# Kernel optimization log

Hardware: AMD Instinct MI355X
Metric: run time of the kernel (lower is better)

Reference implementation:

```python
import jax, jax.numpy as jnp
import numpy as np

H = 1024   # GRU hidden size
Z = 1024   # latent z dim
A = 4      # action dim
F = 30     # number of expert MLPs / max horizon
DIN = Z + H      # 2048, expert MLP input
DH = 512         # expert MLP hidden
EIN = H + 94     # evalMLP input (belief + pos/ori one-hot)
EH = 512
EOUT = 94


def setup_inputs() -> dict:
    key = jax.random.key(0)
    ks = jax.random.split(key, 20)
    s = 0.02
    inp = {
        "b_t": jax.random.normal(ks[0], (1, H), jnp.float32),
        "a_t": jax.random.normal(ks[1], (F, A), jnp.float32),
        "z_tp1_pos": jax.random.normal(ks[2], (F, Z), jnp.float32),
        "z_tp1_neg": jax.random.normal(ks[3], (F, Z), jnp.float32),
        "init_pos_ori": jax.random.uniform(ks[4], (1, 94), jnp.float32),
        # action GRU params (PyTorch layout: W_ih (3H, A), W_hh (3H, H))
        "gru_Wih": jax.random.normal(ks[5], (3 * H, A), jnp.float32) * s,
        "gru_Whh": jax.random.normal(ks[6], (3 * H, H), jnp.float32) * s,
        "gru_bih": jax.random.normal(ks[7], (3 * H,), jnp.float32) * s,
        "gru_bhh": jax.random.normal(ks[8], (3 * H,), jnp.float32) * s,
        # 30 stacked expert MLPs: Linear(DIN,DH)+ReLU+Linear(DH,1)
        "mlp_W1": jax.random.normal(ks[9], (F, DIN, DH), jnp.float32) * s,
        "mlp_b1": jax.random.normal(ks[10], (F, DH), jnp.float32) * s,
        "mlp_W2": jax.random.normal(ks[11], (F, DH, 1), jnp.float32) * s,
        "mlp_b2": jax.random.normal(ks[12], (F, 1), jnp.float32) * s,
        # evalMLP: Linear(EIN,EH)+ReLU+Linear(EH,EOUT)+sigmoid
        "eval_W1": jax.random.normal(ks[13], (EIN, EH), jnp.float32) * s,
        "eval_b1": jax.random.normal(ks[14], (EH,), jnp.float32) * s,
        "eval_W2": jax.random.normal(ks[15], (EH, EOUT), jnp.float32) * s,
        "eval_b2": jax.random.normal(ks[16], (EOUT,), jnp.float32) * s,
        "f": F,
    }
    return inp


def _gru(x, h0, Wih, Whh, bih, bhh):
    # x: (T, A), h0: (H,) -> outputs (T, H). PyTorch nn.GRU cell math.
    def step(h, xt):
        gi = Wih @ xt + bih          # (3H,)
        gh = Whh @ h + bhh           # (3H,)
        ir, iz, inn = jnp.split(gi, 3)
        hr, hz, hn = jnp.split(gh, 3)
        r = jax.nn.sigmoid(ir + hr)
        z = jax.nn.sigmoid(iz + hz)
        n = jnp.tanh(inn + r * hn)
        h_new = (1.0 - z) * n + z * h
        return h_new, h_new
    _, hs = jax.lax.scan(step, h0, x)
    return hs


def _experts(x, W1, b1, W2, b2, f):
    # x: (f, DIN); expert i applied to row i only (grouped batch-1 GEMMs).
    h = jax.nn.relu(jnp.einsum('fi,fih->fh', x, W1[:f]) + b1[:f])
    return jnp.einsum('fh,fho->fo', h, W2[:f]) + b2[:f]   # (f, 1) logits


def reference(b_t, a_t, z_tp1_pos, z_tp1_neg, init_pos_ori,
              gru_Wih, gru_Whh, gru_bih, gru_bhh,
              mlp_W1, mlp_b1, mlp_W2, mlp_b2,
              eval_W1, eval_b1, eval_W2, eval_b2, f):
    a_gru = _gru(a_t[:f], b_t[0], gru_Wih, gru_Whh, gru_bih, gru_bhh)  # (f, H)
    z_pos = jnp.concatenate([z_tp1_pos[:f], a_gru], axis=1)           # (f, Z+H)
    pred_positive = _experts(z_pos, mlp_W1, mlp_b1, mlp_W2, mlp_b2, f)
    z_neg = jnp.concatenate([z_tp1_neg[:f], a_gru], axis=1)
    pred_negative = _experts(z_neg, mlp_W1, mlp_b1, mlp_W2, mlp_b2, f)
    # eval branch uses b_t.detach()
    eval_in = jnp.concatenate([jax.lax.stop_gradient(b_t), init_pos_ori], axis=1)
    eh = jax.nn.relu(eval_in @ eval_W1 + eval_b1)
    pred_xytheta = jax.nn.sigmoid(eh @ eval_W2 + eval_b2)             # (1, 94)
    return pred_positive, pred_negative, pred_xytheta
```

## Files before the change

### kernel.cpp

```cpp
#include <hip/hip_runtime.h>
#include <math.h>

constexpr int kH    = 1024;
constexpr int kZ    = 1024;
constexpr int kA    = 4;
constexpr int kF    = 30;
constexpr int kDIN  = 2048;
constexpr int kDH   = 512;
constexpr int kEIN  = 1118;
constexpr int kEH   = 512;
constexpr int kEOUT = 94;

constexpr int GRU_NB  = 64;
constexpr int EXP_PRT = 8;

constexpr size_t HACC_OFF = 0;
constexpr size_t EHA_OFF  = HACC_OFF + (size_t)kF * 2 * EXP_PRT * kDH;
constexpr size_t TAG_OFF  = EHA_OFF + (size_t)8 * kEH;

__device__ __forceinline__ float sigmoidf_(float x) { return 1.0f / (1.0f + __expf(-x)); }

__device__ __forceinline__ float wave_reduce(float v) {
#pragma unroll
  for (int off = 32; off > 0; off >>= 1) v += __shfl_down(v, off, 64);
  return v;
}

__device__ __forceinline__ unsigned long long tag_ld(const unsigned long long* p) {
  return __hip_atomic_load(p, __ATOMIC_RELAXED, __HIP_MEMORY_SCOPE_AGENT);
}
__device__ __forceinline__ void tag_st(unsigned long long* p, unsigned long long v) {
  __hip_atomic_store(p, v, __ATOMIC_RELAXED, __HIP_MEMORY_SCOPE_AGENT);
}

#define PIN4(v) asm volatile("" : "+v"((v).x), "+v"((v).y), "+v"((v).z), "+v"((v).w))

__global__ __launch_bounds__(512, 2) void gru64(const float* __restrict__ Whh,
                                                const float* __restrict__ bhh,
                                                const float* __restrict__ Wih,
                                                const float* __restrict__ bih,
                                                const float* __restrict__ a_t,
                                                const float* __restrict__ b_t,
                                                unsigned long long* __restrict__ tagbuf,
                                                const int* __restrict__ fptr) {
  const int bid  = blockIdx.x;
  const int tid  = threadIdx.x;
  const int wave = tid >> 6;
  const int lane = tid & 63;
  const int f    = *fptr;

  const int jb = bid * 16;
  const int j0 = jb + wave;
  const int j1 = jb + wave + 8;

  __shared__ float gis[kF][16][3];
  __shared__ __align__(16) float hs[kH];

  const float4* W4 = (const float4*)Whh;
  float4 wr0[4], wz0[4], wn0[4], wr1[4], wz1[4], wn1[4];
#pragma unroll
  for (int i = 0; i < 4; i++) {
    wr0[i] = W4[(size_t)j0 * 256 + i * 64 + lane];
    wz0[i] = W4[(size_t)(j0 + kH) * 256 + i * 64 + lane];
    wn0[i] = W4[(size_t)(j0 + 2 * kH) * 256 + i * 64 + lane];
    wr1[i] = W4[(size_t)j1 * 256 + i * 64 + lane];
    wz1[i] = W4[(size_t)(j1 + kH) * 256 + i * 64 + lane];
    wn1[i] = W4[(size_t)(j1 + 2 * kH) * 256 + i * 64 + lane];
  }
#pragma unroll
  for (int i = 0; i < 4; i++) {
    PIN4(wr0[i]); PIN4(wz0[i]); PIN4(wn0[i]);
    PIN4(wr1[i]); PIN4(wz1[i]); PIN4(wn1[i]);
  }
  const float b0r = bhh[j0], b0z = bhh[j0 + kH], b0n = bhh[j0 + 2 * kH];
  const float b1r = bhh[j1], b1z = bhh[j1 + kH], b1n = bhh[j1 + 2 * kH];

  for (int idx = tid; idx < kF * 16 * 3; idx += 512) {
    int t = idx / 48;
    int rem = idx - t * 48;
    int w = rem / 3, g = rem - w * 3;
    int r = jb + w + g * kH;
    float acc = bih[r];
    const float* wih = Wih + (size_t)r * kA;
    const float* at  = a_t + (size_t)t * kA;
#pragma unroll
    for (int k = 0; k < kA; k++) acc += wih[k] * at[k];
    gis[t][w][g] = acc;
  }
  __syncthreads();

  const float4* hs4 = (const float4*)hs;
  for (int t = 0; t < f; t++) {
    if (t == 0) {
      hs[tid]       = b_t[tid];
      hs[tid + 512] = b_t[tid + 512];
    } else {
      const unsigned long long* tg = tagbuf + (size_t)(t - 1) * kH;
      const unsigned want = (unsigned)t;
      unsigned long long v0 = tag_ld(tg + tid);
      unsigned long long v1 = tag_ld(tg + tid + 512);
      while ((unsigned)(v0 >> 32) != want) v0 = tag_ld(tg + tid);
      while ((unsigned)(v1 >> 32) != want) v1 = tag_ld(tg + tid + 512);
      hs[tid]       = __uint_as_float((unsigned)v0);
      hs[tid + 512] = __uint_as_float((unsigned)v1);
    }
    __syncthreads();

    float a0r = 0.f, a0z = 0.f, a0n = 0.f, a1r = 0.f, a1z = 0.f, a1n = 0.f;
#pragma unroll
    for (int i = 0; i < 4; i++) {
      float4 h4 = hs4[i * 64 + lane];
      a0r += wr0[i].x * h4.x + wr0[i].y * h4.y + wr0[i].z * h4.z + wr0[i].w * h4.w;
      a0z += wz0[i].x * h4.x + wz0[i].y * h4.y + wz0[i].z * h4.z + wz0[i].w * h4.w;
      a0n += wn0[i].x * h4.x + wn0[i].y * h4.y + wn0[i].z * h4.z + wn0[i].w * h4.w;
      a1r += wr1[i].x * h4.x + wr1[i].y * h4.y + wr1[i].z * h4.z + wr1[i].w * h4.w;
      a1z += wz1[i].x * h4.x + wz1[i].y * h4.y + wz1[i].z * h4.z + wz1[i].w * h4.w;
      a1n += wn1[i].x * h4.x + wn1[i].y * h4.y + wn1[i].z * h4.z + wn1[i].w * h4.w;
    }
    a0r = wave_reduce(a0r); a0z = wave_reduce(a0z); a0n = wave_reduce(a0n);
    a1r = wave_reduce(a1r); a1z = wave_reduce(a1z); a1n = wave_reduce(a1n);

    if (lane == 0) {
      float rg = sigmoidf_(gis[t][wave][0] + a0r + b0r);
      float zg = sigmoidf_(gis[t][wave][1] + a0z + b0z);
      float ng = tanhf(gis[t][wave][2] + rg * (a0n + b0n));
      float h0 = (1.0f - zg) * ng + zg * hs[j0];
      rg = sigmoidf_(gis[t][wave + 8][0] + a1r + b1r);
      zg = sigmoidf_(gis[t][wave + 8][1] + a1z + b1z);
      ng = tanhf(gis[t][wave + 8][2] + rg * (a1n + b1n));
      float h1 = (1.0f - zg) * ng + zg * hs[j1];

      const unsigned long long tg = (unsigned long long)(unsigned)(t + 1) << 32;
      tag_st(tagbuf + (size_t)t * kH + j0, tg | (unsigned long long)__float_as_uint(h0));
      tag_st(tagbuf + (size_t)t * kH + j1, tg | (unsigned long long)__float_as_uint(h1));
    }
    __syncthreads();
  }
}

__global__ __launch_bounds__(512) void experts(const float* __restrict__ zpos,
                                               const float* __restrict__ zneg,
                                               const unsigned long long* __restrict__ tagbuf,
                                               const float* __restrict__ W1,
                                               const float* __restrict__ b_t,
                                               const float* __restrict__ ipo,
                                               const float* __restrict__ eW1,
                                               float* __restrict__ hacc,
                                               float* __restrict__ ehacc,
                                               const int* __restrict__ fptr) {
  const int bid = blockIdx.x;
  const int tid = threadIdx.x;
  const int f   = *fptr;

  if (bid < kF * EXP_PRT) {
    __shared__ float xs_p[256];
    __shared__ float xs_n[256];
    int e = bid >> 3, part = bid & 7;
    if (e >= f) return;

    if (part < 4) {
      int r0 = part * 256;
      if (tid < 256) {
        xs_p[tid] = zpos[(size_t)e * kZ + r0 + tid];
        xs_n[tid] = zneg[(size_t)e * kZ + r0 + tid];
      }
      __syncthreads();
      float ap = 0.f, an = 0.f;
      const float* w = W1 + ((size_t)e * kDIN + r0) * kDH + tid;
#pragma unroll 8
      for (int r = 0; r < 256; r++) {
        float wv = w[(size_t)r * kDH];
        ap += xs_p[r] * wv;
        an += xs_n[r] * wv;
      }
      hacc[(((size_t)e * 2 + 0) * EXP_PRT + part) * kDH + tid] = ap;
      hacc[(((size_t)e * 2 + 1) * EXP_PRT + part) * kDH + tid] = an;
    } else {
      int r0 = (part - 4) * 256;
      if (tid < 256)
        xs_p[tid] = __uint_as_float((unsigned)tagbuf[(size_t)e * kH + r0 + tid]);
      __syncthreads();
      float a = 0.f;
      const float* w = W1 + ((size_t)e * kDIN + kZ + r0) * kDH + tid;
#pragma unroll 8
      for (int r = 0; r < 256; r++) a += xs_p[r] * w[(size_t)r * kDH];
      hacc[(((size_t)e * 2 + 0) * EXP_PRT + part) * kDH + tid] = a;
      hacc[(((size_t)e * 2 + 1) * EXP_PRT + part) * kDH + tid] = a;
    }
  } else {
    __shared__ float evs[140];
    int part = bid - kF * EXP_PRT;
    int r0 = part * 140;
    int nr = min(140, kEIN - r0);
    if (tid < nr) {
      int r = r0 + tid;
      evs[tid] = (r < kH) ? b_t[r] : ipo[r - kH];
    }
    __syncthreads();
    float acc = 0.f;
    const float* w = eW1 + (size_t)r0 * kEH + tid;
    for (int r = 0; r < nr; r++) acc += evs[r] * w[(size_t)r * kEH];
    ehacc[(size_t)part * kEH + tid] = acc;
  }
}

__global__ __launch_bounds__(512) void stage2(const float* __restrict__ hacc,
                                              const float* __restrict__ ehacc,
                                              const float* __restrict__ b1,
                                              const float* __restrict__ W2,
                                              const float* __restrict__ b2,
                                              const float* __restrict__ eb1,
                                              const float* __restrict__ eW2,
                                              const float* __restrict__ eb2,
                                              float* __restrict__ out,
                                              const int* __restrict__ fptr) {
  int b = blockIdx.x;
  int tid = threadIdx.x;
  int f = *fptr;
  if (b < kF) {
    int i = b;
    if (i >= f) return;
    float sp = 0.f, sn = 0.f;
#pragma unroll
    for (int p = 0; p < EXP_PRT; p++) {
      sp += hacc[(((size_t)i * 2 + 0) * EXP_PRT + p) * kDH + tid];
      sn += hacc[(((size_t)i * 2 + 1) * EXP_PRT + p) * kDH + tid];
    }
    float bias = b1[(size_t)i * kDH + tid];
    float hp = fmaxf(sp + bias, 0.f);
    float hn = fmaxf(sn + bias, 0.f);
    float w = W2[(size_t)i * kDH + tid];
    float pp = wave_reduce(hp * w);
    float pn = wave_reduce(hn * w);
    __shared__ float redp[8];
    __shared__ float redn[8];
    int wave = tid >> 6, lane = tid & 63;
    if (lane == 0) { redp[wave] = pp; redn[wave] = pn; }
    __syncthreads();
    if (tid == 0) {
      float s0 = 0.f, s1 = 0.f;
#pragma unroll
      for (int k = 0; k < 8; k++) { s0 += redp[k]; s1 += redn[k]; }
      out[i] = s0 + b2[i];
      out[f + i] = s1 + b2[i];
    }
  } else {
    __shared__ float ehs[kEH];
    {
      float s = eb1[tid];
#pragma unroll
      for (int p = 0; p < 8; p++) s += ehacc[(size_t)p * kEH + tid];
      ehs[tid] = fmaxf(s, 0.f);
    }
    __syncthreads();
    if (tid < kEOUT) {
      float acc = eb2[tid];
      for (int h = 0; h < kEH; h++) acc += ehs[h] * eW2[(size_t)h * kEOUT + tid];
      out[2 * f + tid] = sigmoidf_(acc);
    }
  }
}

extern "C" void kernel_launch(void* const* d_in, const int* in_sizes, int n_in,
                              void* d_out, int out_size, void* d_ws, size_t ws_size,
                              hipStream_t stream) {
  const float* b_t  = (const float*)d_in[0];
  const float* a_t  = (const float*)d_in[1];
  const float* zpos = (const float*)d_in[2];
  const float* zneg = (const float*)d_in[3];
  const float* ipo  = (const float*)d_in[4];
  const float* gWih = (const float*)d_in[5];
  const float* gWhh = (const float*)d_in[6];
  const float* gbih = (const float*)d_in[7];
  const float* gbhh = (const float*)d_in[8];
  const float* mW1  = (const float*)d_in[9];
  const float* mb1  = (const float*)d_in[10];
  const float* mW2  = (const float*)d_in[11];
  const float* mb2  = (const float*)d_in[12];
  const float* eW1  = (const float*)d_in[13];
  const float* eb1  = (const float*)d_in[14];
  const float* eW2  = (const float*)d_in[15];
  const float* eb2  = (const float*)d_in[16];
  const int*   fptr = (const int*)d_in[17];

  float* ws     = (float*)d_ws;
  float* hacc   = ws + HACC_OFF;
  float* ehacc  = ws + EHA_OFF;
  unsigned long long* tagbuf = (unsigned long long*)(ws + TAG_OFF);
  float* out    = (float*)d_out;

  gru64<<<GRU_NB, 512, 0, stream>>>(gWhh, gbhh, gWih, gbih, a_t, b_t, tagbuf, fptr);

  experts<<<kF * EXP_PRT + 8, 512, 0, stream>>>(zpos, zneg, tagbuf, mW1, b_t, ipo, eW1,
                                                hacc, ehacc, fptr);

  stage2<<<kF + 1, 512, 0, stream>>>(hacc, ehacc, mb1, mW2, mb2, eb1, eW2, eb2, out, fptr);
}
```

Before: 354.7 us.

## Double-buffer GRU hidden state, vectorize tag polling, reload weights each step

The GRU step loop now double-buffers the shared hidden state, so the trailing barrier can go. Each thread polls two adjacent tagged values with one 16-byte load, issued in inline asm with an sc1 cache bypass and a short sleep between retries. Each wave now owns two adjacent output rows so the poll layout matches. Whh is no longer pinned in registers but reloaded from global memory every timestep. This cuts register pressure but adds per-step global or cache traffic on the serial critical path.

```diff
diff --git a/kernel.cpp b/kernel.cpp
--- a/kernel.cpp
+++ b/kernel.cpp
@@ -18,6 +18,8 @@
 constexpr size_t EHA_OFF  = HACC_OFF + (size_t)kF * 2 * EXP_PRT * kDH;
 constexpr size_t TAG_OFF  = EHA_OFF + (size_t)8 * kEH;
 
+typedef unsigned uint4e __attribute__((ext_vector_type(4)));
+
 __device__ __forceinline__ float sigmoidf_(float x) { return 1.0f / (1.0f + __expf(-x)); }
 
 __device__ __forceinline__ float wave_reduce(float v) {
@@ -26,14 +28,16 @@
   return v;
 }
 
-__device__ __forceinline__ unsigned long long tag_ld(const unsigned long long* p) {
-  return __hip_atomic_load(p, __ATOMIC_RELAXED, __HIP_MEMORY_SCOPE_AGENT);
-}
 __device__ __forceinline__ void tag_st(unsigned long long* p, unsigned long long v) {
   __hip_atomic_store(p, v, __ATOMIC_RELAXED, __HIP_MEMORY_SCOPE_AGENT);
 }
 
-#define PIN4(v) asm volatile("" : "+v"((v).x), "+v"((v).y), "+v"((v).z), "+v"((v).w))
+__device__ __forceinline__ uint4e poll16(const uint4e* p) {
+  uint4e v;
+  asm volatile("global_load_dwordx4 %0, %1, off sc1\n\ts_waitcnt vmcnt(0)"
+               : "=v"(v) : "v"(p) : "memory");
+  return v;
+}
 
 __global__ __launch_bounds__(512, 2) void gru64(const float* __restrict__ Whh,
                                                 const float* __restrict__ bhh,
@@ -50,30 +54,11 @@
   const int f    = *fptr;
 
   const int jb = bid * 16;
-  const int j0 = jb + wave;
-  const int j1 = jb + wave + 8;
+  const int j0 = jb + 2 * wave;
+  const int j1 = j0 + 1;
 
   __shared__ float gis[kF][16][3];
-  __shared__ __align__(16) float hs[kH];
-
-  const float4* W4 = (const float4*)Whh;
-  float4 wr0[4], wz0[4], wn0[4], wr1[4], wz1[4], wn1[4];
-#pragma unroll
-  for (int i = 0; i < 4; i++) {
-    wr0[i] = W4[(size_t)j0 * 256 + i * 64 + lane];
-    wz0[i] = W4[(size_t)(j0 + kH) * 256 + i * 64 + lane];
-    wn0[i] = W4[(size_t)(j0 + 2 * kH) * 256 + i * 64 + lane];
-    wr1[i] = W4[(size_t)j1 * 256 + i * 64 + lane];
-    wz1[i] = W4[(size_t)(j1 + kH) * 256 + i * 64 + lane];
-    wn1[i] = W4[(size_t)(j1 + 2 * kH) * 256 + i * 64 + lane];
-  }
-#pragma unroll
-  for (int i = 0; i < 4; i++) {
-    PIN4(wr0[i]); PIN4(wz0[i]); PIN4(wn0[i]);
-    PIN4(wr1[i]); PIN4(wz1[i]); PIN4(wn1[i]);
-  }
-  const float b0r = bhh[j0], b0z = bhh[j0 + kH], b0n = bhh[j0 + 2 * kH];
-  const float b1r = bhh[j1], b1z = bhh[j1 + kH], b1n = bhh[j1 + 2 * kH];
+  __shared__ __align__(16) float hsd[2][kH];
 
   for (int idx = tid; idx < kF * 16 * 3; idx += 512) {
     int t = idx / 48;
@@ -89,23 +74,41 @@
   }
   __syncthreads();
 
-  const float4* hs4 = (const float4*)hs;
+  const float4* W4 = (const float4*)Whh;
+  const float b0r = bhh[j0], b0z = bhh[j0 + kH], b0n = bhh[j0 + 2 * kH];
+  const float b1r = bhh[j1], b1z = bhh[j1 + kH], b1n = bhh[j1 + 2 * kH];
+
   for (int t = 0; t < f; t++) {
+    float* hsb = hsd[t & 1];
+
+    float4 wr0[4], wz0[4], wn0[4], wr1[4], wz1[4], wn1[4];
+#pragma unroll
+    for (int i = 0; i < 4; i++) {
+      wr0[i] = W4[(size_t)j0 * 256 + i * 64 + lane];
+      wz0[i] = W4[(size_t)(j0 + kH) * 256 + i * 64 + lane];
+      wn0[i] = W4[(size_t)(j0 + 2 * kH) * 256 + i * 64 + lane];
+      wr1[i] = W4[(size_t)j1 * 256 + i * 64 + lane];
+      wz1[i] = W4[(size_t)(j1 + kH) * 256 + i * 64 + lane];
+      wn1[i] = W4[(size_t)(j1 + 2 * kH) * 256 + i * 64 + lane];
+    }
+
     if (t == 0) {
-      hs[tid]       = b_t[tid];
-      hs[tid + 512] = b_t[tid + 512];
+      hsb[tid]       = b_t[tid];
+      hsb[tid + 512] = b_t[tid + 512];
     } else {
-      const unsigned long long* tg = tagbuf + (size_t)(t - 1) * kH;
+      const uint4e* tg = (const uint4e*)(tagbuf + (size_t)(t - 1) * kH);
       const unsigned want = (unsigned)t;
-      unsigned long long v0 = tag_ld(tg + tid);
-      unsigned long long v1 = tag_ld(tg + tid + 512);
-      while ((unsigned)(v0 >> 32) != want) v0 = tag_ld(tg + tid);
-      while ((unsigned)(v1 >> 32) != want) v1 = tag_ld(tg + tid + 512);
-      hs[tid]       = __uint_as_float((unsigned)v0);
-      hs[tid + 512] = __uint_as_float((unsigned)v1);
+      uint4e v = poll16(tg + tid);
+      while (v.y != want || v.w != want) {
+        __builtin_amdgcn_s_sleep(1);
+        v = poll16(tg + tid);
+      }
+      hsb[2 * tid]     = __uint_as_float(v.x);
+      hsb[2 * tid + 1] = __uint_as_float(v.z);
     }
     __syncthreads();
 
+    const float4* hs4 = (const float4*)hsb;
     float a0r = 0.f, a0z = 0.f, a0n = 0.f, a1r = 0.f, a1z = 0.f, a1n = 0.f;
 #pragma unroll
     for (int i = 0; i < 4; i++) {
@@ -121,20 +124,19 @@
     a1r = wave_reduce(a1r); a1z = wave_reduce(a1z); a1n = wave_reduce(a1n);
 
     if (lane == 0) {
-      float rg = sigmoidf_(gis[t][wave][0] + a0r + b0r);
-      float zg = sigmoidf_(gis[t][wave][1] + a0z + b0z);
-      float ng = tanhf(gis[t][wave][2] + rg * (a0n + b0n));
-      float h0 = (1.0f - zg) * ng + zg * hs[j0];
-      rg = sigmoidf_(gis[t][wave + 8][0] + a1r + b1r);
-      zg = sigmoidf_(gis[t][wave + 8][1] + a1z + b1z);
-      ng = tanhf(gis[t][wave + 8][2] + rg * (a1n + b1n));
-      float h1 = (1.0f - zg) * ng + zg * hs[j1];
+      float rg = sigmoidf_(gis[t][2 * wave][0] + a0r + b0r);
+      float zg = sigmoidf_(gis[t][2 * wave][1] + a0z + b0z);
+      float ng = tanhf(gis[t][2 * wave][2] + rg * (a0n + b0n));
+      float h0 = (1.0f - zg) * ng + zg * hsb[j0];
+      rg = sigmoidf_(gis[t][2 * wave + 1][0] + a1r + b1r);
+      zg = sigmoidf_(gis[t][2 * wave + 1][1] + a1z + b1z);
+      ng = tanhf(gis[t][2 * wave + 1][2] + rg * (a1n + b1n));
+      float h1 = (1.0f - zg) * ng + zg * hsb[j1];
 
       const unsigned long long tg = (unsigned long long)(unsigned)(t + 1) << 32;
       tag_st(tagbuf + (size_t)t * kH + j0, tg | (unsigned long long)__float_as_uint(h0));
       tag_st(tagbuf + (size_t)t * kH + j1, tg | (unsigned long long)__float_as_uint(h1));
     }
-    __syncthreads();
   }
 }
 
```

Measured after the change: 365.5 us. 3.1% more time.
